# Performance work log

Hardware: AMD Instinct MI355X
Metric: run time of the kernel (lower is better)

## Reference

```python
import jax, jax.numpy as jnp
import numpy as np

B, L, D = 8, 512, 512
VOCAB = 50257
N_CLASSES = 225          # ceil(sqrt(50257))
N_PER_CLASS = 224        # ceil(50257 / 225)


def _glorot(key, shape, fan_in, fan_out):
    s = np.sqrt(6.0 / (fan_in + fan_out)).astype(np.float32)
    return jax.random.uniform(key, shape, jnp.float32, -s, s)


def setup_inputs() -> dict:
    key = jax.random.key(0)
    k = jax.random.split(key, 4)
    x = jax.random.normal(k[0], (B, L, D), jnp.float32)
    target = jax.random.randint(k[1], (B, L), 0, VOCAB)
    W1 = _glorot(k[2], (D, N_CLASSES), D, N_CLASSES)
    b1 = jnp.zeros((N_CLASSES,), jnp.float32)
    W2 = _glorot(k[3], (N_CLASSES, D, N_PER_CLASS), D, N_PER_CLASS)
    b2 = jnp.zeros((N_CLASSES, N_PER_CLASS), jnp.float32)
    return {"x": x, "target": target, "W1": W1, "b1": b1, "W2": W2, "b2": b2}


def reference(x, target, W1, b1, W2, b2):
    # Theano h_softmax with target given: returns p(target | x), shape [B, L, 1].
    xf = x.reshape(-1, D)                      # [N, D]
    t = target.reshape(-1)                     # [N]
    cls = t // N_PER_CLASS                     # class id per token
    idx = t % N_PER_CLASS                      # within-class id per token

    class_p = jax.nn.softmax(xf @ W1 + b1, axis=-1)          # [N, C]

    W2g = W2[cls]                                            # gather: [N, D, O]
    in_logits = jnp.einsum('nd,ndo->no', xf, W2g) + b2[cls]  # [N, O]
    in_p = jax.nn.softmax(in_logits, axis=-1)                # [N, O]

    n = jnp.arange(xf.shape[0])
    p = class_p[n, cls] * in_p[n, idx]                       # [N]
    return p.reshape(B, L, 1)
```

## Files before the change

kernel.cpp:

```cpp
#include <hip/hip_runtime.h>
#include <cmath>

typedef _Float16 half8 __attribute__((ext_vector_type(8)));
typedef float f32x4 __attribute__((ext_vector_type(4)));

constexpr int D   = 512;
constexpr int NC  = 225;
constexpr int NPC = 224;
constexpr int N1  = 256;
constexpr int TB  = 32;

constexpr int WS_NCHUNK = 0;
constexpr int WS_CHUNK  = 16;
constexpr int WS_ORDER  = 4096;
constexpr int WS_B1P    = 8192;
constexpr int WS_W1H    = 8448;
constexpr int WS_W1L    = 73984;
constexpr int WS_XH     = 139520;
constexpr int WS_XL     = 1188096;
constexpr int WS_STAT   = 2236672;

__device__ __forceinline__ void f16split(float v, _Float16& h, _Float16& l) {
    _Float16 hh = (_Float16)v;
    float hf = (float)hh;
    if (fabsf(hf) < 6.104e-5f) { hh = (_Float16)0.f; hf = 0.f; }
    h = hh;
    l = (_Float16)((v - hf) * 2048.0f);
}

__global__ __launch_bounds__(256) void k_prep_pre(
    const float* __restrict__ x, const float* __restrict__ W1,
    const float* __restrict__ b1, const int* __restrict__ target,
    int* __restrict__ ws, int ntok)
{
    const int bid = blockIdx.x, tid = threadIdx.x;
    if (bid == 0) {
        __shared__ int h[256], sc[256], sc2[256], cur[NC];
        h[tid] = 0;
        __syncthreads();
        for (int n = tid; n < ntok; n += 256) atomicAdd(&h[target[n] / NPC], 1);
        __syncthreads();
        const int hv = h[tid];
        sc[tid] = hv; __syncthreads();
        for (int o = 1; o < 256; o <<= 1) {
            int a = (tid >= o) ? sc[tid - o] : 0;
            __syncthreads();
            sc[tid] += a;
            __syncthreads();
        }
        const int start = sc[tid] - hv;
        const int nch = (tid < NC) ? (hv + TB - 1) / TB : 0;
        sc2[tid] = nch; __syncthreads();
        for (int o = 1; o < 256; o <<= 1) {
            int a = (tid >= o) ? sc2[tid - o] : 0;
            __syncthreads();
            sc2[tid] += a;
            __syncthreads();
        }
        const int nch2 = sc2[255];
        if (tid < NC) {
            cur[tid] = start;
            const int cb = sc2[tid] - nch;
            for (int j = 0; j < nch; ++j) {
                for (int q = 0; q < 2; ++q) {
                    const int e = WS_CHUNK + (((cb + j) * 2) + q) * 4;
                    ws[e + 0] = tid;
                    ws[e + 1] = start + j * TB;
                    ws[e + 2] = min(TB, hv - j * TB);
                    ws[e + 3] = q;
                }
            }
        }
        const int P1C = ntok / TB;
        if (tid < P1C) {
            for (int q = 0; q < 2; ++q) {
                const int e = WS_CHUNK + (nch2 * 2 + tid * 2 + q) * 4;
                ws[e + 0] = -1;
                ws[e + 1] = tid * TB;
                ws[e + 2] = TB;
                ws[e + 3] = q;
            }
        }
        if (tid == 0) ws[WS_NCHUNK] = nch2 * 2 + P1C * 2;
        __syncthreads();
        for (int n = tid; n < ntok; n += 256) {
            const int c = target[n] / NPC;
            const int pos = atomicAdd(&cur[c], 1);
            ws[WS_ORDER + pos] = n;
        }
        return;
    }
    const int pb = bid - 1;
    _Float16* xh  = (_Float16*)(ws + WS_XH);
    _Float16* xl  = (_Float16*)(ws + WS_XL);
    _Float16* w1h = (_Float16*)(ws + WS_W1H);
    _Float16* w1l = (_Float16*)(ws + WS_W1L);
    const int XBLK = (ntok * D) / (256 * 8);
    if (pb < XBLK) {
        const int base = (pb * 256 + tid) * 8;
        const float4 a = *(const float4*)(x + base);
        const float4 b = *(const float4*)(x + base + 4);
        const float v[8] = {a.x, a.y, a.z, a.w, b.x, b.y, b.z, b.w};
        half8 hv, lv;
        #pragma unroll
        for (int j = 0; j < 8; ++j) {
            _Float16 hq, lq;
            f16split(v[j], hq, lq);
            hv[j] = hq; lv[j] = lq;
        }
        *(half8*)(xh + base) = hv;
        *(half8*)(xl + base) = lv;
    } else if (pb < XBLK + 64) {
        const int oi = ((pb - XBLK) * 256 + tid) * 8;
        const int c = oi >> 9, k0 = oi & 511;
        half8 hv, lv;
        #pragma unroll
        for (int j = 0; j < 8; ++j) {
            const float v = (c < NC) ? W1[(size_t)(k0 + j) * NC + c] : 0.f;
            _Float16 hq, lq;
            f16split(v, hq, lq);
            hv[j] = hq; lv[j] = lq;
        }
        *(half8*)(w1h + oi) = hv;
        *(half8*)(w1l + oi) = lv;
    } else {
        float* b1p = (float*)ws + WS_B1P;
        if (tid < N1) b1p[tid] = (tid < NC) ? b1[tid] : 0.f;
    }
}

#define LW(buf, kk)                                                              \
    do {                                                                         \
        _Pragma("unroll")                                                        \
        for (int mi = 0; mi < 2; ++mi) if (tval[mi]) {                           \
            const float* p_ = wpm[mi] + (size_t)((kk) + l4 * 8) * NPC;           \
            _Pragma("unroll")                                                    \
            for (int j = 0; j < 8; ++j) buf[mi][j] = p_[(size_t)j * NPC];        \
        }                                                                        \
    } while (0)

#define LX(bh, bl, kk)                                                           \
    do {                                                                         \
        _Pragma("unroll")                                                        \
        for (int n = 0; n < 2; ++n) if (n < ntiles) {                            \
            bh[n] = *(const half8*)(xh + xoff[n] + (kk) + l4 * 8);               \
            bl[n] = *(const half8*)(xl + xoff[n] + (kk) + l4 * 8);               \
        }                                                                        \
    } while (0)

#define LA(ah, al, kk)                                                           \
    do {                                                                         \
        _Pragma("unroll")                                                        \
        for (int mi = 0; mi < 2; ++mi) if (tval[mi]) {                           \
            const int col_ = (mt0 + mi) * 16 + l15;                              \
            ah[mi] = *(const half8*)(w1h + (size_t)col_ * D + (kk) + l4 * 8);    \
            al[mi] = *(const half8*)(w1l + (size_t)col_ * D + (kk) + l4 * 8);    \
        }                                                                        \
    } while (0)

#define PROCW(buf, bh, bl)                                                       \
    do {                                                                         \
        _Pragma("unroll")                                                        \
        for (int mi = 0; mi < 2; ++mi) if (tval[mi]) {                           \
            half8 Ah_, Al_;                                                      \
            _Pragma("unroll")                                                    \
            for (int j = 0; j < 8; ++j) {                                        \
                _Float16 hq_, lq_;                                               \
                f16split(buf[mi][j], hq_, lq_);                                  \
                Ah_[j] = hq_; Al_[j] = lq_;                                      \
            }                                                                    \
            _Pragma("unroll")                                                    \
            for (int n = 0; n < 2; ++n) if (n < ntiles) {                        \
                accA[mi][n] = __builtin_amdgcn_mfma_f32_16x16x32_f16(Ah_, bh[n], accA[mi][n], 0, 0, 0); \
                accB[mi][n] = __builtin_amdgcn_mfma_f32_16x16x32_f16(Ah_, bl[n], accB[mi][n], 0, 0, 0); \
                accB[mi][n] = __builtin_amdgcn_mfma_f32_16x16x32_f16(Al_, bh[n], accB[mi][n], 0, 0, 0); \
            }                                                                    \
        }                                                                        \
    } while (0)

#define PROCA(ah, al, bh, bl)                                                    \
    do {                                                                         \
        _Pragma("unroll")                                                        \
        for (int mi = 0; mi < 2; ++mi) if (tval[mi]) {                           \
            _Pragma("unroll")                                                    \
            for (int n = 0; n < 2; ++n) if (n < ntiles) {                        \
                accA[mi][n] = __builtin_amdgcn_mfma_f32_16x16x32_f16(ah[mi], bh[n], accA[mi][n], 0, 0, 0); \
                accB[mi][n] = __builtin_amdgcn_mfma_f32_16x16x32_f16(ah[mi], bl[n], accB[mi][n], 0, 0, 0); \
                accB[mi][n] = __builtin_amdgcn_mfma_f32_16x16x32_f16(al[mi], bh[n], accB[mi][n], 0, 0, 0); \
            }                                                                    \
        }                                                                        \
    } while (0)

template <bool PH2>
__device__ __forceinline__ void run_chunk(
    const int* __restrict__ target, const float* __restrict__ W2c,
    const float* __restrict__ bsrc,
    const _Float16* __restrict__ w1h, const _Float16* __restrict__ w1l,
    const _Float16* __restrict__ xh, const _Float16* __restrict__ xl,
    int* __restrict__ ws, int* __restrict__ stok,
    int start, int cnt, int ch)
{
    constexpr int NREAL = PH2 ? NPC : NC;
    const int tid = threadIdx.x, w = tid >> 6, lane = tid & 63;
    const int l15 = lane & 15, l4 = lane >> 4;

    if (tid < TB)
        stok[tid] = PH2 ? ws[WS_ORDER + start + min(tid, cnt - 1)] : (start + tid);
    __syncthreads();

    const int ntiles = (cnt + 15) >> 4;
    int xoff[2];
    xoff[0] = stok[l15] * D;
    xoff[1] = stok[16 + l15] * D;

    const int mt0 = ch * 8 + w * 2;
    bool tval[2];
    tval[0] = (mt0 * 16) < NREAL;
    tval[1] = ((mt0 + 1) * 16) < NREAL;

    f32x4 accA[2][2] = {}, accB[2][2] = {};

    if constexpr (PH2) {
        const float* wpm[2];
        #pragma unroll
        for (int mi = 0; mi < 2; ++mi) {
            const int col = (mt0 + mi) * 16 + l15;
            wpm[mi] = W2c + min(col, NPC - 1);
        }
        float wra[2][8], wrb[2][8];
        half8 xha[2], xla[2], xhb[2], xlb[2];
        LW(wra, 0); LX(xha, xla, 0);
        for (int k0 = 0; k0 < D; k0 += 64) {
            LW(wrb, k0 + 32); LX(xhb, xlb, k0 + 32);
            PROCW(wra, xha, xla);
            if (k0 + 64 < D) { LW(wra, k0 + 64); LX(xha, xla, k0 + 64); }
            PROCW(wrb, xhb, xlb);
        }
    } else {
        half8 aha[2], ala[2], ahb[2], alb[2];
        half8 xha[2], xla[2], xhb[2], xlb[2];
        LA(aha, ala, 0); LX(xha, xla, 0);
        for (int k0 = 0; k0 < D; k0 += 64) {
            LA(ahb, alb, k0 + 32); LX(xhb, xlb, k0 + 32);
            PROCA(aha, ala, xha, xla);
            if (k0 + 64 < D) { LA(aha, ala, k0 + 64); LX(xha, xla, k0 + 64); }
            PROCA(ahb, alb, xhb, xlb);
        }
    }

    float* stat = (float*)ws + WS_STAT;
    #pragma unroll
    for (int n = 0; n < 2; ++n) {
        if (n < ntiles) {
            const int tok = stok[n * 16 + l15];
            const int tt  = target[tok];
            const int tcol = PH2 ? (tt % NPC) : (tt / NPC);
            float vals[2][4];
            float mx = -1e30f;
            #pragma unroll
            for (int mi = 0; mi < 2; ++mi) {
                const int col0 = (mt0 + mi) * 16 + l4 * 4;
                const int bcol = PH2 ? min(col0, NPC - 4) : col0;
                const float4 bv = *(const float4*)(bsrc + bcol);
                #pragma unroll
                for (int r = 0; r < 4; ++r) {
                    const float v = accA[mi][n][r] + accB[mi][n][r] * (1.f / 2048.f) + (&bv.x)[r];
                    vals[mi][r] = v;
                    if (col0 + r < NREAL) mx = fmaxf(mx, v);
                }
            }
            mx = fmaxf(mx, __shfl_xor(mx, 16, 64));
            mx = fmaxf(mx, __shfl_xor(mx, 32, 64));
            float s = 0.f, e = 0.f;
            #pragma unroll
            for (int mi = 0; mi < 2; ++mi) {
                const int col0 = (mt0 + mi) * 16 + l4 * 4;
                #pragma unroll
                for (int r = 0; r < 4; ++r) {
                    const int cr = col0 + r;
                    if (cr < NREAL) {
                        const float ex = __expf(vals[mi][r] - mx);
                        s += ex;
                        if (cr == tcol) e = ex;
                    }
                }
            }
            s += __shfl_xor(s, 16, 64); s += __shfl_xor(s, 32, 64);
            e += __shfl_xor(e, 16, 64); e += __shfl_xor(e, 32, 64);
            if (l4 == 0) {
                const int g = (PH2 ? 8 : 0) + ch * 4 + w;
                *(float4*)(stat + (size_t)tok * 64 + g * 4) = {mx, s, e, 0.f};
            }
        }
    }
}

__global__ __launch_bounds__(256, 4) void k_main(
    const int* __restrict__ target, const float* __restrict__ W2,
    const float* __restrict__ b2, int* __restrict__ ws)
{
    __shared__ int stok[TB];
    const int bid = blockIdx.x;
    if (bid >= ws[WS_NCHUNK]) return;
    const int4 ce = *(const int4*)(ws + WS_CHUNK + bid * 4);
    const _Float16* w1h = (const _Float16*)(ws + WS_W1H);
    const _Float16* w1l = (const _Float16*)(ws + WS_W1L);
    const _Float16* xh  = (const _Float16*)(ws + WS_XH);
    const _Float16* xl  = (const _Float16*)(ws + WS_XL);
    if (ce.x >= 0) {
        run_chunk<true>(target, W2 + (size_t)ce.x * D * NPC, b2 + ce.x * NPC,
                        w1h, w1l, xh, xl, ws, stok, ce.y, ce.z, ce.w);
    } else {
        run_chunk<false>(target, nullptr, (const float*)ws + WS_B1P,
                         w1h, w1l, xh, xl, ws, stok, ce.y, ce.z, ce.w);
    }
}

__global__ __launch_bounds__(256) void k_combine(const int* __restrict__ ws,
                                                 float* __restrict__ out, int ntok) {
    const int n = blockIdx.x * 256 + threadIdx.x;
    if (n >= ntok) return;
    const float4* st = (const float4*)((const float*)ws + WS_STAT) + (size_t)n * 16;
    float p[2];
    #pragma unroll
    for (int ph = 0; ph < 2; ++ph) {
        float M = -1e30f;
        #pragma unroll
        for (int g = 0; g < 8; ++g) M = fmaxf(M, st[ph * 8 + g].x);
        float S = 0.f, E = 0.f;
        #pragma unroll
        for (int g = 0; g < 8; ++g) {
            const float4 q = st[ph * 8 + g];
            const float sc = __expf(q.x - M);
            S += q.y * sc;
            E += q.z * sc;
        }
        p[ph] = E / S;
    }
    out[n] = p[0] * p[1];
}

extern "C" void kernel_launch(void* const* d_in, const int* in_sizes, int n_in,
                              void* d_out, int out_size, void* d_ws, size_t ws_size,
                              hipStream_t stream) {
    const float* x      = (const float*)d_in[0];
    const int*   target = (const int*)  d_in[1];
    const float* W1     = (const float*)d_in[2];
    const float* b1     = (const float*)d_in[3];
    const float* W2     = (const float*)d_in[4];
    const float* b2     = (const float*)d_in[5];
    float* out = (float*)d_out;
    int*   wsi = (int*)d_ws;

    const int ntok = in_sizes[1];
    const int maxgrid = 2 * (NC + ntok / TB) + 2 * (ntok / TB);
    const int pregrid = 1 + (ntok * D) / (256 * 8) + 64 + 1;

    k_prep_pre<<<pregrid, 256, 0, stream>>>(x, W1, b1, target, wsi, ntok);
    k_main    <<<maxgrid, 256, 0, stream>>>(target, W2, b2, wsi);
    k_combine <<<(ntok + 255) / 256, 256, 0, stream>>>(wsi, out, ntok);
}
```

Baseline: 55.57 us.

## Split K dimension across two wave groups with shared-memory reduction in main kernel

Doubles the block to 512 threads and assigns each half of the waves one half of the D=512 reduction dimension for the MFMA dot products. The upper group writes its partial accumulators to shared memory, and after a barrier the lower group adds them and runs the softmax-statistics epilogue. The aim is more parallelism and memory-level concurrency per chunk, shortening the serial K loop. The cost is an extra block-wide sync, a 16 KB LDS buffer that may limit occupancy, and half the waves sitting idle during the epilogue.

```diff
diff --git a/kernel.cpp b/kernel.cpp
--- a/kernel.cpp
+++ b/kernel.cpp
@@ -197,12 +197,14 @@
     const float* __restrict__ bsrc,
     const _Float16* __restrict__ w1h, const _Float16* __restrict__ w1l,
     const _Float16* __restrict__ xh, const _Float16* __restrict__ xl,
-    int* __restrict__ ws, int* __restrict__ stok,
+    int* __restrict__ ws, int* __restrict__ stok, f32x4* __restrict__ redbuf,
     int start, int cnt, int ch)
 {
     constexpr int NREAL = PH2 ? NPC : NC;
     const int tid = threadIdx.x, w = tid >> 6, lane = tid & 63;
+    const int wq = w & 3, kq = w >> 2;
     const int l15 = lane & 15, l4 = lane >> 4;
+    const int kbase = kq * 256;
 
     if (tid < TB)
         stok[tid] = PH2 ? ws[WS_ORDER + start + min(tid, cnt - 1)] : (start + tid);
@@ -213,7 +215,7 @@
     xoff[0] = stok[l15] * D;
     xoff[1] = stok[16 + l15] * D;
 
-    const int mt0 = ch * 8 + w * 2;
+    const int mt0 = ch * 8 + wq * 2;
     bool tval[2];
     tval[0] = (mt0 * 16) < NREAL;
     tval[1] = ((mt0 + 1) * 16) < NREAL;
@@ -229,24 +231,53 @@
         }
         float wra[2][8], wrb[2][8];
         half8 xha[2], xla[2], xhb[2], xlb[2];
-        LW(wra, 0); LX(xha, xla, 0);
-        for (int k0 = 0; k0 < D; k0 += 64) {
+        LW(wra, kbase); LX(xha, xla, kbase);
+        for (int k0 = kbase; k0 < kbase + 256; k0 += 64) {
             LW(wrb, k0 + 32); LX(xhb, xlb, k0 + 32);
             PROCW(wra, xha, xla);
-            if (k0 + 64 < D) { LW(wra, k0 + 64); LX(xha, xla, k0 + 64); }
+            if (k0 + 64 < kbase + 256) { LW(wra, k0 + 64); LX(xha, xla, k0 + 64); }
             PROCW(wrb, xhb, xlb);
         }
     } else {
         half8 aha[2], ala[2], ahb[2], alb[2];
         half8 xha[2], xla[2], xhb[2], xlb[2];
-        LA(aha, ala, 0); LX(xha, xla, 0);
-        for (int k0 = 0; k0 < D; k0 += 64) {
+        LA(aha, ala, kbase); LX(xha, xla, kbase);
+        for (int k0 = kbase; k0 < kbase + 256; k0 += 64) {
             LA(ahb, alb, k0 + 32); LX(xhb, xlb, k0 + 32);
             PROCA(aha, ala, xha, xla);
-            if (k0 + 64 < D) { LA(aha, ala, k0 + 64); LX(xha, xla, k0 + 64); }
+            if (k0 + 64 < kbase + 256) { LA(aha, ala, k0 + 64); LX(xha, xla, k0 + 64); }
             PROCA(ahb, alb, xhb, xlb);
         }
     }
+
+    f32x4 red[2][2];
+    #pragma unroll
+    for (int mi = 0; mi < 2; ++mi)
+        #pragma unroll
+        for (int n = 0; n < 2; ++n) {
+            red[mi][n][0] = accA[mi][n][0] + accB[mi][n][0] * (1.f / 2048.f);
+            red[mi][n][1] = accA[mi][n][1] + accB[mi][n][1] * (1.f / 2048.f);
+            red[mi][n][2] = accA[mi][n][2] + accB[mi][n][2] * (1.f / 2048.f);
+            red[mi][n][3] = accA[mi][n][3] + accB[mi][n][3] * (1.f / 2048.f);
+        }
+
+    if (kq == 1) {
+        #pragma unroll
+        for (int mi = 0; mi < 2; ++mi)
+            #pragma unroll
+            for (int n = 0; n < 2; ++n)
+                redbuf[(((wq * 2 + mi) * 2) + n) * 64 + lane] = red[mi][n];
+    }
+    __syncthreads();
+    if (kq != 0) return;
+    #pragma unroll
+    for (int mi = 0; mi < 2; ++mi)
+        #pragma unroll
+        for (int n = 0; n < 2; ++n) {
+            const f32x4 o = redbuf[(((wq * 2 + mi) * 2) + n) * 64 + lane];
+            red[mi][n][0] += o[0]; red[mi][n][1] += o[1];
+            red[mi][n][2] += o[2]; red[mi][n][3] += o[3];
+        }
 
     float* stat = (float*)ws + WS_STAT;
     #pragma unroll
@@ -264,7 +295,7 @@
                 const float4 bv = *(const float4*)(bsrc + bcol);
                 #pragma unroll
                 for (int r = 0; r < 4; ++r) {
-                    const float v = accA[mi][n][r] + accB[mi][n][r] * (1.f / 2048.f) + (&bv.x)[r];
+                    const float v = red[mi][n][r] + (&bv.x)[r];
                     vals[mi][r] = v;
                     if (col0 + r < NREAL) mx = fmaxf(mx, v);
                 }
@@ -288,18 +319,19 @@
             s += __shfl_xor(s, 16, 64); s += __shfl_xor(s, 32, 64);
             e += __shfl_xor(e, 16, 64); e += __shfl_xor(e, 32, 64);
             if (l4 == 0) {
-                const int g = (PH2 ? 8 : 0) + ch * 4 + w;
+                const int g = (PH2 ? 8 : 0) + ch * 4 + wq;
                 *(float4*)(stat + (size_t)tok * 64 + g * 4) = {mx, s, e, 0.f};
             }
         }
     }
 }
 
-__global__ __launch_bounds__(256, 4) void k_main(
+__global__ __launch_bounds__(512, 8) void k_main(
     const int* __restrict__ target, const float* __restrict__ W2,
     const float* __restrict__ b2, int* __restrict__ ws)
 {
     __shared__ int stok[TB];
+    __shared__ f32x4 redbuf[16 * 64];
     const int bid = blockIdx.x;
     if (bid >= ws[WS_NCHUNK]) return;
     const int4 ce = *(const int4*)(ws + WS_CHUNK + bid * 4);
@@ -309,10 +341,10 @@
     const _Float16* xl  = (const _Float16*)(ws + WS_XL);
     if (ce.x >= 0) {
         run_chunk<true>(target, W2 + (size_t)ce.x * D * NPC, b2 + ce.x * NPC,
-                        w1h, w1l, xh, xl, ws, stok, ce.y, ce.z, ce.w);
+                        w1h, w1l, xh, xl, ws, stok, redbuf, ce.y, ce.z, ce.w);
     } else {
         run_chunk<false>(target, nullptr, (const float*)ws + WS_B1P,
-                         w1h, w1l, xh, xl, ws, stok, ce.y, ce.z, ce.w);
+                         w1h, w1l, xh, xl, ws, stok, redbuf, ce.y, ce.z, ce.w);
     }
 }
 
@@ -357,6 +389,6 @@
     const int pregrid = 1 + (ntok * D) / (256 * 8) + 64 + 1;
 
     k_prep_pre<<<pregrid, 256, 0, stream>>>(x, W1, b1, target, wsi, ntok);
-    k_main    <<<maxgrid, 256, 0, stream>>>(target, W2, b2, wsi);
+    k_main    <<<maxgrid, 512, 0, stream>>>(target, W2, b2, wsi);
     k_combine <<<(ntok + 255) / 256, 256, 0, stream>>>(wsi, out, ntok);
 }
```

Result: slower. 220.2 us (+296.2%).

## Stage W2 tiles through LDS with async global_load_lds double buffering

Applied to the files above, without the earlier changes.

The phase-2 (within-class) GEMM no longer reads W2 directly from global memory with strided per-lane scalar loads. Each block now copies a contiguous 32x112 fp32 slice of W2 into a double-buffered LDS tile using global_load_lds, then reads it from LDS for the f16 split and MFMA. The column split also changes from 8 tiles per chunk (with clamping) to 7 tiles of 16 columns per chunk. The aim is coalesced, asynchronous W2 fetches that overlap with compute, at the cost of 28KB of LDS per block and a barrier per k-step, which may reduce occupancy.

```diff
diff --git a/kernel.cpp b/kernel.cpp
--- a/kernel.cpp
+++ b/kernel.cpp
@@ -129,16 +129,6 @@
     }
 }
 
-#define LW(buf, kk)                                                              \
-    do {                                                                         \
-        _Pragma("unroll")                                                        \
-        for (int mi = 0; mi < 2; ++mi) if (tval[mi]) {                           \
-            const float* p_ = wpm[mi] + (size_t)((kk) + l4 * 8) * NPC;           \
-            _Pragma("unroll")                                                    \
-            for (int j = 0; j < 8; ++j) buf[mi][j] = p_[(size_t)j * NPC];        \
-        }                                                                        \
-    } while (0)
-
 #define LX(bh, bl, kk)                                                           \
     do {                                                                         \
         _Pragma("unroll")                                                        \
@@ -155,26 +145,6 @@
             const int col_ = (mt0 + mi) * 16 + l15;                              \
             ah[mi] = *(const half8*)(w1h + (size_t)col_ * D + (kk) + l4 * 8);    \
             al[mi] = *(const half8*)(w1l + (size_t)col_ * D + (kk) + l4 * 8);    \
-        }                                                                        \
-    } while (0)
-
-#define PROCW(buf, bh, bl)                                                       \
-    do {                                                                         \
-        _Pragma("unroll")                                                        \
-        for (int mi = 0; mi < 2; ++mi) if (tval[mi]) {                           \
-            half8 Ah_, Al_;                                                      \
-            _Pragma("unroll")                                                    \
-            for (int j = 0; j < 8; ++j) {                                        \
-                _Float16 hq_, lq_;                                               \
-                f16split(buf[mi][j], hq_, lq_);                                  \
-                Ah_[j] = hq_; Al_[j] = lq_;                                      \
-            }                                                                    \
-            _Pragma("unroll")                                                    \
-            for (int n = 0; n < 2; ++n) if (n < ntiles) {                        \
-                accA[mi][n] = __builtin_amdgcn_mfma_f32_16x16x32_f16(Ah_, bh[n], accA[mi][n], 0, 0, 0); \
-                accB[mi][n] = __builtin_amdgcn_mfma_f32_16x16x32_f16(Ah_, bl[n], accB[mi][n], 0, 0, 0); \
-                accB[mi][n] = __builtin_amdgcn_mfma_f32_16x16x32_f16(Al_, bh[n], accB[mi][n], 0, 0, 0); \
-            }                                                                    \
         }                                                                        \
     } while (0)
 
@@ -191,24 +161,139 @@
         }                                                                        \
     } while (0)
 
-template <bool PH2>
-__device__ __forceinline__ void run_chunk(
+__device__ __forceinline__ void run_p2(
     const int* __restrict__ target, const float* __restrict__ W2c,
     const float* __restrict__ bsrc,
+    const _Float16* __restrict__ xh, const _Float16* __restrict__ xl,
+    int* __restrict__ ws, int* __restrict__ stok, float* __restrict__ wtile,
+    int start, int cnt, int ch)
+{
+    const int tid = threadIdx.x, w = tid >> 6, lane = tid & 63;
+    const int l15 = lane & 15, l4 = lane >> 4;
+
+    if (tid < TB) stok[tid] = ws[WS_ORDER + start + min(tid, cnt - 1)];
+    __syncthreads();
+
+    const int ntiles = (cnt + 15) >> 4;
+    int xoff[2];
+    xoff[0] = stok[l15] * D;
+    xoff[1] = stok[16 + l15] * D;
+
+    const int lt0 = w * 2;
+    bool tval[2];
+    tval[0] = (lt0 < 7);
+    tval[1] = (lt0 + 1 < 7);
+
+    f32x4 accA[2][2] = {}, accB[2][2] = {};
+
+    const char* gW = (const char*)W2c + ch * 448;
+
+    #define STAGE(buf, kt)                                                          \
+        do {                                                                        \
+            const char* gb_ = gW + (size_t)(kt) * 28672;                            \
+            _Pragma("unroll")                                                       \
+            for (int i_ = 0; i_ < 4; ++i_) {                                        \
+                const int ii_ = w + i_ * 4;                                         \
+                if (ii_ < 14) {                                                     \
+                    const int flat_ = ii_ * 1024 + lane * 16;                       \
+                    const int row_ = flat_ / 448, off_ = flat_ % 448;               \
+                    __builtin_amdgcn_global_load_lds(                               \
+                        (const __attribute__((address_space(1))) uint32_t*)         \
+                            (gb_ + (size_t)row_ * 896 + off_),                      \
+                        (__attribute__((address_space(3))) uint32_t*)               \
+                            (wtile + (buf) * 3584 + ii_ * 256),                     \
+                        16, 0, 0);                                                  \
+                }                                                                   \
+            }                                                                       \
+        } while (0)
+
+    STAGE(0, 0);
+    __syncthreads();
+
+    for (int kt = 0; kt < 16; ++kt) {
+        const int cur = kt & 1;
+        if (kt + 1 < 16) STAGE(cur ^ 1, kt + 1);
+        const int k0 = kt * 32;
+        half8 Bh[2], Bl[2];
+        LX(Bh, Bl, k0);
+        #pragma unroll
+        for (int mi = 0; mi < 2; ++mi) if (tval[mi]) {
+            half8 Ah, Al;
+            const float* wrow = wtile + cur * 3584 + (lt0 + mi) * 16 + l15;
+            #pragma unroll
+            for (int j = 0; j < 8; ++j) {
+                _Float16 hq, lq;
+                f16split(wrow[(l4 * 8 + j) * 112], hq, lq);
+                Ah[j] = hq; Al[j] = lq;
+            }
+            #pragma unroll
+            for (int n = 0; n < 2; ++n) if (n < ntiles) {
+                accA[mi][n] = __builtin_amdgcn_mfma_f32_16x16x32_f16(Ah, Bh[n], accA[mi][n], 0, 0, 0);
+                accB[mi][n] = __builtin_amdgcn_mfma_f32_16x16x32_f16(Ah, Bl[n], accB[mi][n], 0, 0, 0);
+                accB[mi][n] = __builtin_amdgcn_mfma_f32_16x16x32_f16(Al, Bh[n], accB[mi][n], 0, 0, 0);
+            }
+        }
+        __syncthreads();
+    }
+    #undef STAGE
+
+    float* stat = (float*)ws + WS_STAT;
+    #pragma unroll
+    for (int n = 0; n < 2; ++n) {
+        if (n < ntiles) {
+            const int tok = stok[n * 16 + l15];
+            const int tcol = target[tok] % NPC;
+            float vals[2][4];
+            float mx = -1e30f;
+            #pragma unroll
+            for (int mi = 0; mi < 2; ++mi) if (tval[mi]) {
+                const int col0 = (ch * 7 + lt0 + mi) * 16 + l4 * 4;
+                const float4 bv = *(const float4*)(bsrc + col0);
+                #pragma unroll
+                for (int r = 0; r < 4; ++r) {
+                    const float v = accA[mi][n][r] + accB[mi][n][r] * (1.f / 2048.f) + (&bv.x)[r];
+                    vals[mi][r] = v;
+                    mx = fmaxf(mx, v);
+                }
+            }
+            mx = fmaxf(mx, __shfl_xor(mx, 16, 64));
+            mx = fmaxf(mx, __shfl_xor(mx, 32, 64));
+            float s = 0.f, e = 0.f;
+            #pragma unroll
+            for (int mi = 0; mi < 2; ++mi) if (tval[mi]) {
+                const int col0 = (ch * 7 + lt0 + mi) * 16 + l4 * 4;
+                #pragma unroll
+                for (int r = 0; r < 4; ++r) {
+                    const float ex = __expf(vals[mi][r] - mx);
+                    s += ex;
+                    if (col0 + r == tcol) e = ex;
+                }
+            }
+            s += __shfl_xor(s, 16, 64); s += __shfl_xor(s, 32, 64);
+            e += __shfl_xor(e, 16, 64); e += __shfl_xor(e, 32, 64);
+            if (l4 == 0) {
+                const int g = 8 + ch * 4 + w;
+                *(float4*)(stat + (size_t)tok * 64 + g * 4) = {mx, s, e, 0.f};
+            }
+        }
+    }
+}
+
+__device__ __forceinline__ void run_p1(
+    const int* __restrict__ target, const float* __restrict__ bsrc,
     const _Float16* __restrict__ w1h, const _Float16* __restrict__ w1l,
     const _Float16* __restrict__ xh, const _Float16* __restrict__ xl,
     int* __restrict__ ws, int* __restrict__ stok,
     int start, int cnt, int ch)
 {
-    constexpr int NREAL = PH2 ? NPC : NC;
+    constexpr int NREAL = NC;
     const int tid = threadIdx.x, w = tid >> 6, lane = tid & 63;
     const int l15 = lane & 15, l4 = lane >> 4;
 
-    if (tid < TB)
-        stok[tid] = PH2 ? ws[WS_ORDER + start + min(tid, cnt - 1)] : (start + tid);
+    if (tid < TB) stok[tid] = start + tid;
     __syncthreads();
 
-    const int ntiles = (cnt + 15) >> 4;
+    const int ntiles = 2;
     int xoff[2];
     xoff[0] = stok[l15] * D;
     xoff[1] = stok[16 + l15] * D;
@@ -220,77 +305,55 @@
 
     f32x4 accA[2][2] = {}, accB[2][2] = {};
 
-    if constexpr (PH2) {
-        const float* wpm[2];
-        #pragma unroll
-        for (int mi = 0; mi < 2; ++mi) {
-            const int col = (mt0 + mi) * 16 + l15;
-            wpm[mi] = W2c + min(col, NPC - 1);
-        }
-        float wra[2][8], wrb[2][8];
-        half8 xha[2], xla[2], xhb[2], xlb[2];
-        LW(wra, 0); LX(xha, xla, 0);
-        for (int k0 = 0; k0 < D; k0 += 64) {
-            LW(wrb, k0 + 32); LX(xhb, xlb, k0 + 32);
-            PROCW(wra, xha, xla);
-            if (k0 + 64 < D) { LW(wra, k0 + 64); LX(xha, xla, k0 + 64); }
-            PROCW(wrb, xhb, xlb);
-        }
-    } else {
-        half8 aha[2], ala[2], ahb[2], alb[2];
-        half8 xha[2], xla[2], xhb[2], xlb[2];
-        LA(aha, ala, 0); LX(xha, xla, 0);
-        for (int k0 = 0; k0 < D; k0 += 64) {
-            LA(ahb, alb, k0 + 32); LX(xhb, xlb, k0 + 32);
-            PROCA(aha, ala, xha, xla);
-            if (k0 + 64 < D) { LA(aha, ala, k0 + 64); LX(xha, xla, k0 + 64); }
-            PROCA(ahb, alb, xhb, xlb);
-        }
+    half8 aha[2], ala[2], ahb[2], alb[2];
+    half8 xha[2], xla[2], xhb[2], xlb[2];
+    LA(aha, ala, 0); LX(xha, xla, 0);
+    for (int k0 = 0; k0 < D; k0 += 64) {
+        LA(ahb, alb, k0 + 32); LX(xhb, xlb, k0 + 32);
+        PROCA(aha, ala, xha, xla);
+        if (k0 + 64 < D) { LA(aha, ala, k0 + 64); LX(xha, xla, k0 + 64); }
+        PROCA(ahb, alb, xhb, xlb);
     }
 
     float* stat = (float*)ws + WS_STAT;
     #pragma unroll
     for (int n = 0; n < 2; ++n) {
-        if (n < ntiles) {
-            const int tok = stok[n * 16 + l15];
-            const int tt  = target[tok];
-            const int tcol = PH2 ? (tt % NPC) : (tt / NPC);
-            float vals[2][4];
-            float mx = -1e30f;
-            #pragma unroll
-            for (int mi = 0; mi < 2; ++mi) {
-                const int col0 = (mt0 + mi) * 16 + l4 * 4;
-                const int bcol = PH2 ? min(col0, NPC - 4) : col0;
-                const float4 bv = *(const float4*)(bsrc + bcol);
-                #pragma unroll
-                for (int r = 0; r < 4; ++r) {
-                    const float v = accA[mi][n][r] + accB[mi][n][r] * (1.f / 2048.f) + (&bv.x)[r];
-                    vals[mi][r] = v;
-                    if (col0 + r < NREAL) mx = fmaxf(mx, v);
+        const int tok = stok[n * 16 + l15];
+        const int tcol = target[tok] / NPC;
+        float vals[2][4];
+        float mx = -1e30f;
+        #pragma unroll
+        for (int mi = 0; mi < 2; ++mi) {
+            const int col0 = (mt0 + mi) * 16 + l4 * 4;
+            const float4 bv = *(const float4*)(bsrc + col0);
+            #pragma unroll
+            for (int r = 0; r < 4; ++r) {
+                const float v = accA[mi][n][r] + accB[mi][n][r] * (1.f / 2048.f) + (&bv.x)[r];
+                vals[mi][r] = v;
+                if (col0 + r < NREAL) mx = fmaxf(mx, v);
+            }
+        }
+        mx = fmaxf(mx, __shfl_xor(mx, 16, 64));
+        mx = fmaxf(mx, __shfl_xor(mx, 32, 64));
+        float s = 0.f, e = 0.f;
+        #pragma unroll
+        for (int mi = 0; mi < 2; ++mi) {
+            const int col0 = (mt0 + mi) * 16 + l4 * 4;
+            #pragma unroll
+            for (int r = 0; r < 4; ++r) {
+                const int cr = col0 + r;
+                if (cr < NREAL) {
+                    const float ex = __expf(vals[mi][r] - mx);
+                    s += ex;
+                    if (cr == tcol) e = ex;
                 }
             }
-            mx = fmaxf(mx, __shfl_xor(mx, 16, 64));
-            mx = fmaxf(mx, __shfl_xor(mx, 32, 64));
-            float s = 0.f, e = 0.f;
-            #pragma unroll
-            for (int mi = 0; mi < 2; ++mi) {
-                const int col0 = (mt0 + mi) * 16 + l4 * 4;
-                #pragma unroll
-                for (int r = 0; r < 4; ++r) {
-                    const int cr = col0 + r;
-                    if (cr < NREAL) {
-                        const float ex = __expf(vals[mi][r] - mx);
-                        s += ex;
-                        if (cr == tcol) e = ex;
-                    }
-                }
-            }
-            s += __shfl_xor(s, 16, 64); s += __shfl_xor(s, 32, 64);
-            e += __shfl_xor(e, 16, 64); e += __shfl_xor(e, 32, 64);
-            if (l4 == 0) {
-                const int g = (PH2 ? 8 : 0) + ch * 4 + w;
-                *(float4*)(stat + (size_t)tok * 64 + g * 4) = {mx, s, e, 0.f};
-            }
+        }
+        s += __shfl_xor(s, 16, 64); s += __shfl_xor(s, 32, 64);
+        e += __shfl_xor(e, 16, 64); e += __shfl_xor(e, 32, 64);
+        if (l4 == 0) {
+            const int g = ch * 4 + w;
+            *(float4*)(stat + (size_t)tok * 64 + g * 4) = {mx, s, e, 0.f};
         }
     }
 }
@@ -299,6 +362,7 @@
     const int* __restrict__ target, const float* __restrict__ W2,
     const float* __restrict__ b2, int* __restrict__ ws)
 {
+    __shared__ float wtile[2 * 3584];
     __shared__ int stok[TB];
     const int bid = blockIdx.x;
     if (bid >= ws[WS_NCHUNK]) return;
@@ -308,11 +372,11 @@
     const _Float16* xh  = (const _Float16*)(ws + WS_XH);
     const _Float16* xl  = (const _Float16*)(ws + WS_XL);
     if (ce.x >= 0) {
-        run_chunk<true>(target, W2 + (size_t)ce.x * D * NPC, b2 + ce.x * NPC,
-                        w1h, w1l, xh, xl, ws, stok, ce.y, ce.z, ce.w);
+        run_p2(target, W2 + (size_t)ce.x * D * NPC, b2 + ce.x * NPC,
+               xh, xl, ws, stok, wtile, ce.y, ce.z, ce.w);
     } else {
-        run_chunk<false>(target, nullptr, (const float*)ws + WS_B1P,
-                         w1h, w1l, xh, xl, ws, stok, ce.y, ce.z, ce.w);
+        run_p1(target, (const float*)ws + WS_B1P, w1h, w1l,
+               xh, xl, ws, stok, ce.y, ce.z, ce.w);
     }
 }
 
```

Result: no change. 54.95 us (-1.1%).
